# Performance work log

Measured on AMD Instinct MI355X. Metric: run time of the kernel, lower is better.

## Reference

```python
import jax, jax.numpy as jnp
import numpy as np

B, N, P = 256, 12, 66
DN = 1024   # node_feature_size
DE = 1024   # edge_feature_size
D = 512     # message_size
DIMS = [3 * D, 1024, 512]  # shared trunk dims; heads differ only in out classes
C_LR, C_CR, C_MR = 9, 3, 5


def _mlp(x, Ws, bs):
    # ReLU MLP, no activation on final layer (eval mode: dropout is identity)
    for i, (W, b) in enumerate(zip(Ws, bs)):
        x = x @ W + b
        if i < len(Ws) - 1:
            x = jax.nn.relu(x)
    return x


def _head_params(key, out_dim):
    dims = DIMS + [out_dim]
    Ws, bs = [], []
    for i in range(len(dims) - 1):
        key, k = jax.random.split(key)
        Ws.append(jax.random.normal(k, (dims[i], dims[i + 1]), jnp.float32) * (1.0 / np.sqrt(dims[i])))
        bs.append(jnp.zeros((dims[i + 1],), jnp.float32))
    return Ws, bs


def setup_inputs() -> dict:
    key = jax.random.key(0)
    ks = jax.random.split(key, 12)
    inp = {
        'node_features': jax.random.normal(ks[0], (B, N, DN), jnp.float32),
        'edge_features': jax.random.normal(ks[1], (B, N, N, DE), jnp.float32),
        'edge_embeddings': jax.random.normal(ks[2], (B, N, N, D), jnp.float32),
        'pairs': jax.random.randint(ks[3], (B, P, 2), 0, N),
        'num_rels': jax.random.randint(ks[4], (B,), 0, P + 1),
        'W_node': jax.random.normal(ks[5], (DN, D), jnp.float32) * (1.0 / np.sqrt(DN)),
        'b_node': jnp.zeros((D,), jnp.float32),
        'W_edge': jax.random.normal(ks[6], (DE, D), jnp.float32) * (1.0 / np.sqrt(DE)),
        'b_edge': jnp.zeros((D,), jnp.float32),
    }
    for name, cdim, k in (('lr', C_LR, ks[7]), ('cr', C_CR, ks[8]), ('mr', C_MR, ks[9])):
        Ws, bs = _head_params(k, cdim)
        for i in range(3):
            inp[f'{name}_W{i}'] = Ws[i]
            inp[f'{name}_b{i}'] = bs[i]
    return inp


def reference(node_features, edge_features, edge_embeddings, pairs, num_rels,
              W_node, b_node, W_edge, b_edge,
              lr_W0, lr_b0, lr_W1, lr_b1, lr_W2, lr_b2,
              cr_W0, cr_b0, cr_W1, cr_b1, cr_W2, cr_b2,
              mr_W0, mr_b0, mr_W1, mr_b1, mr_W2, mr_b2):
    # feature resize linears
    nf = node_features @ W_node + b_node        # [B,N,D]
    ef = edge_features @ W_edge + b_edge        # [B,N,N,D]

    # vectorized make_classifier_inputs
    i0, i1 = pairs[..., 0], pairs[..., 1]       # [B,P]
    bidx = jnp.arange(nf.shape[0])[:, None]     # [B,1]
    n1 = nf[bidx, i0]                           # [B,P,D]
    n2 = nf[bidx, i1]                           # [B,P,D]
    emb_mean = 0.5 * (edge_embeddings[bidx, i0, i1] + edge_embeddings[bidx, i1, i0])
    feat_mean = 0.5 * (ef[bidx, i0, i1] + ef[bidx, i1, i0])
    e = 0.5 * (emb_mean + feat_mean)            # [B,P,D]
    ci = jnp.concatenate([n1, n2, e], axis=-1)  # [B,P,3D]

    # rows i >= num_rels[b] stay zero (preallocated-zeros semantics)
    valid = (jnp.arange(ci.shape[1])[None, :] < num_rels[:, None])[..., None]
    ci = jnp.where(valid, ci, jnp.zeros((), ci.dtype))

    lr = _mlp(ci, [lr_W0, lr_W1, lr_W2], [lr_b0, lr_b1, lr_b2])
    cr = _mlp(ci, [cr_W0, cr_W1, cr_W2], [cr_b0, cr_b1, cr_b2])
    mr = _mlp(ci, [mr_W0, mr_W1, mr_W2], [mr_b0, mr_b1, mr_b2])
    return lr, cr, mr
```

## Files before the change

### kernel.cpp

```cpp
#include <hip/hip_runtime.h>
#include <stdint.h>

#define BB 256
#define NNODE 12
#define PP 66
#define DNF 1024
#define DEF 1024
#define DD 512
#define MROWS (BB*PP)
#define MNODE (BB*NNODE)
#define MTILES (MROWS/128)

typedef __attribute__((ext_vector_type(8))) short s16x8;
typedef __attribute__((ext_vector_type(4))) float f32x4;
typedef __attribute__((ext_vector_type(8))) unsigned short u16x8;

__device__ __forceinline__ unsigned short f2bf(float f) {
  union { float f; unsigned u; } v; v.f = f;
  return (unsigned short)((v.u + 0x7FFFu + ((v.u >> 16) & 1u)) >> 16);
}
__device__ __forceinline__ float bf2f(unsigned short h) {
  union { unsigned u; float f; } v; v.u = ((unsigned)h) << 16;
  return v.f;
}

__device__ __forceinline__ void gll16(const void* g, void* l) {
  __builtin_amdgcn_global_load_lds(
      (const __attribute__((address_space(1))) void*)g,
      (__attribute__((address_space(3))) void*)l, 16, 0, 0);
}

__global__ __launch_bounds__(256) void k_front(
    const int* __restrict__ nrels, int* __restrict__ offs,
    int* __restrict__ Mv, int2* __restrict__ nodes,
    float* __restrict__ h1part,
    const float* __restrict__ node, unsigned short* __restrict__ node_bf,
    const float* __restrict__ W_node, unsigned short* __restrict__ WnT,
    const float* __restrict__ W_edge, unsigned short* __restrict__ WeT,
    const float* __restrict__ W0a, const float* __restrict__ W0b,
    const float* __restrict__ W0c, unsigned short* __restrict__ W0T,
    const float* __restrict__ W1a, const float* __restrict__ W1b,
    const float* __restrict__ W1c, unsigned short* __restrict__ W1T,
    const float* __restrict__ w2a, const float* __restrict__ w2b,
    const float* __restrict__ w2c,
    const float* __restrict__ b2a, const float* __restrict__ b2b,
    const float* __restrict__ b2c,
    unsigned short* __restrict__ W2T, float* __restrict__ b2pad,
    const float* __restrict__ b0a, const float* __restrict__ b0b,
    const float* __restrict__ b0c, float* __restrict__ b0cat,
    const float* __restrict__ b1a, const float* __restrict__ b1b,
    const float* __restrict__ b1c, float* __restrict__ b1cat,
    const float* __restrict__ b_node, const float* __restrict__ b_edge,
    float* __restrict__ b_ne) {
  __shared__ float tile[64][65];
  const int bid = blockIdx.x, t = threadIdx.x;
  if (bid < 24) {
    const int h = bid >> 3, c = bid & 7;
    const float* b0 = h == 0 ? b0a : (h == 1 ? b0b : b0c);
    const float* W1 = h == 0 ? W1a : (h == 1 ? W1b : W1c);
    const int k0 = c * 128;
    float acc0 = 0.f, acc1 = 0.f;
#pragma unroll 8
    for (int kk = 0; kk < 128; ++kk) {
      const int k = k0 + kk;
      const float bv = fmaxf(b0[k], 0.f);
      acc0 += bv * W1[(size_t)k * 512 + t];
      acc1 += bv * W1[(size_t)k * 512 + t + 256];
    }
    h1part[(size_t)bid * 512 + t] = acc0;
    h1part[(size_t)bid * 512 + t + 256] = acc1;
  } else if (bid == 24) {
    __shared__ int s[256];
    const int val = nrels[t];
    s[t] = val;
    __syncthreads();
    for (int d = 1; d < 256; d <<= 1) {
      int x = (t >= d) ? s[t - d] : 0;
      __syncthreads();
      s[t] += x;
      __syncthreads();
    }
    offs[t] = s[t] - val;
    __syncthreads();
    const int total = s[255];
    if (t == 0) *Mv = total;
    if (t < 128) {
      int cr = total + t;
      if (cr < MROWS) nodes[cr] = make_int2(0, 0);
    }
  } else if (bid < 3097) {
    int i = (bid - 25) * 256 + t;
    float4 v = ((const float4*)node)[i];
    ushort4 o;
    o.x = f2bf(v.x); o.y = f2bf(v.y); o.z = f2bf(v.z); o.w = f2bf(v.w);
    ((ushort4*)node_bf)[i] = o;
  } else if (bid < 4889) {
    int tau = bid - 3097;
    const float* src; unsigned short* dst; int K, N;
    if (tau < 128)       { src = W_node; dst = WnT; K = 1024; N = 512; }
    else if (tau < 256)  { src = W_edge; dst = WeT; K = 1024; N = 512; tau -= 128; }
    else if (tau < 1408) {
      int hh = (tau - 256) / 384; tau = (tau - 256) % 384;
      src = hh == 0 ? W0a : (hh == 1 ? W0b : W0c);
      dst = W0T + (size_t)hh * 1024 * 1536; K = 1536; N = 1024;
    } else {
      int hh = (tau - 1408) / 128; tau = (tau - 1408) % 128;
      src = hh == 0 ? W1a : (hh == 1 ? W1b : W1c);
      dst = W1T + (size_t)hh * 512 * 1024; K = 1024; N = 512;
    }
    const int ntn = N >> 6;
    const int kb = (tau / ntn) * 64, nb = (tau % ntn) * 64;
    const int tx = t & 15, ty = t >> 4;
#pragma unroll
    for (int i = 0; i < 4; i++) {
      float4 v = *(const float4*)&src[(size_t)(kb + ty + 16 * i) * N + nb + tx * 4];
      tile[ty + 16 * i][tx * 4 + 0] = v.x;
      tile[ty + 16 * i][tx * 4 + 1] = v.y;
      tile[ty + 16 * i][tx * 4 + 2] = v.z;
      tile[ty + 16 * i][tx * 4 + 3] = v.w;
    }
    __syncthreads();
    const int wx = t & 7, wy = t >> 3;
#pragma unroll
    for (int i = 0; i < 2; i++) {
      const int n = wy + 32 * i;
      u16x8 o;
#pragma unroll
      for (int j = 0; j < 8; j++) o[j] = f2bf(tile[wx * 8 + j][n]);
      *(u16x8*)&dst[(size_t)(nb + n) * K + kb + wx * 8] = o;
    }
  } else if (bid < 5657) {
    int e = bid - 4889;
    int h = e >> 8, blk = e & 255;
    const int C = (h == 0) ? 9 : ((h == 1) ? 3 : 5);
    const float* W2 = (h == 0) ? w2a : ((h == 1) ? w2b : w2c);
    const float* b2 = (h == 0) ? b2a : ((h == 1) ? b2b : b2c);
    int idx = blk * 256 + t;
    int n = idx >> 9, k = idx & 511;
    W2T[(size_t)h * 65536 + idx] = (n < C) ? f2bf(W2[(size_t)k * C + n]) : (unsigned short)0;
    if (blk == 0 && t < 128)
      b2pad[h * 128 + t] = (t < C) ? b2[t] : 0.f;
  } else if (bid < 5669) {
    int j = bid - 5657;
    const float* b0 = (j < 4) ? b0a : (j < 8 ? b0b : b0c);
    b0cat[j * 256 + t] = b0[(j & 3) * 256 + t];
  } else if (bid < 5675) {
    int j = bid - 5669;
    const float* b1 = (j < 2) ? b1a : (j < 4 ? b1b : b1c);
    b1cat[j * 256 + t] = b1[(j & 1) * 256 + t];
  } else {
    int idx = (bid - 5675) * 256 + t;
    b_ne[idx] = (idx < 512) ? b_node[idx] : b_edge[idx - 512];
  }
}

template <int EPI>
__device__ __forceinline__ void gemm_body(
    unsigned short* sm,
    const unsigned short* __restrict__ A, int ldA,
    const unsigned short* __restrict__ BT, int ldB, int K,
    int Ntiles,
    const float* __restrict__ bias,
    unsigned short* __restrict__ outb, int ldo,
    const unsigned short* __restrict__ em,
    const int* __restrict__ Mvp,
    unsigned short* __restrict__ ci,
    int blocksPerHead, long long aHeadOff, long long bHeadOff,
    long long oHeadOff, int biasHeadOff,
    const int2* __restrict__ nodes,
    const unsigned short* __restrict__ nfa,
    const unsigned short* __restrict__ nfb,
    const int* __restrict__ rmap, int bid) {
  char* smc = (char*)sm;
  const int t = threadIdx.x;
  const int l = t & 63, w = t >> 6;
  const int wm = w >> 1, wn = w & 1;

  int head = 0;
  unsigned short* outp = outb;
  if constexpr (EPI == 3) {
    head = bid / MTILES;
    bid -= head * MTILES;
    A += (size_t)head * MROWS * DD;
    BT += (size_t)head * 128 * DD;
    bias += head * 128;
  } else {
    if (blocksPerHead > 0) {
      head = bid / blocksPerHead;
      bid -= head * blocksPerHead;
      A += (long long)head * aHeadOff;
      BT += (long long)head * bHeadOff;
      bias += head * biasHeadOff;
      outp = outb + (long long)head * oHeadOff;
    }
  }
  const int tn = bid % Ntiles, tm = bid / Ntiles;

  int Mv = MROWS;
  if (Mvp) {
    Mv = *Mvp;
    if (tm * 128 >= Mv) return;
  }

  const int lrow = l >> 3;
  const int scol = (l & 7) ^ lrow;
  const unsigned short* Ap = A + (size_t)(tm * 128 + w * 8 + lrow) * ldA + scol * 8;
  const unsigned short* Bp = BT + (size_t)(tn * 128 + w * 8 + lrow) * ldB + scol * 8;

  f32x4 acc[4][4] = {};
  const int hi = l >> 4, l15 = l & 15, l7 = l & 7;
  const int nk = K >> 6;

  for (int kt = 0; kt < nk; ++kt) {
#pragma unroll
    for (int c = 0; c < 4; ++c) {
      gll16(Ap + (size_t)c * 32 * ldA, smc + c * 4096 + w * 1024);
      gll16(Bp + (size_t)c * 32 * ldB, smc + 16384 + c * 4096 + w * 1024);
    }
    __syncthreads();
#pragma unroll
    for (int kk = 0; kk < 2; ++kk) {
      const int cb = (((kk << 2) + hi) ^ l7) << 4;
      s16x8 af[4], bfr[4];
#pragma unroll
      for (int m = 0; m < 4; m++)
        af[m] = *(const s16x8*)(smc + (wm * 64 + m * 16 + l15) * 128 + cb);
#pragma unroll
      for (int n = 0; n < 4; n++)
        bfr[n] = *(const s16x8*)(smc + 16384 + (wn * 64 + n * 16 + l15) * 128 + cb);
#pragma unroll
      for (int m = 0; m < 4; m++)
#pragma unroll
        for (int n = 0; n < 4; n++)
          asm volatile("v_mfma_f32_16x16x32_bf16 %0, %1, %2, %0"
                       : "+v"(acc[m][n])
                       : "v"(af[m]), "v"(bfr[n]));
    }
    __syncthreads();
    Ap += 64;
    Bp += 64;
  }
  asm volatile("s_nop 7\n\ts_nop 7\n\ts_nop 7" :::);

  if constexpr (EPI == 5) {
    const int se_r = t >> 4;
    const int se_ch = t & 15;
#pragma unroll
    for (int it = 0; it < 8; ++it) {
      const int rr = se_r + (it << 4);
      const int2 nn = nodes[tm * 128 + rr];
      union { unsigned short s[8]; unsigned long long q[2]; } ov;
      u16x8 va = *(const u16x8*)&nfa[(size_t)nn.x * 3072 + tn * 128 + se_ch * 8];
      u16x8 vb = *(const u16x8*)&nfb[(size_t)nn.y * 3072 + tn * 128 + se_ch * 8];
#pragma unroll
      for (int j = 0; j < 8; ++j)
        ov.s[j] = f2bf(bf2f(va[j]) + bf2f(vb[j]));
      const int sch = se_ch ^ ((rr >> 2) & 7);
      *(unsigned long long*)(smc + rr * 256 + (sch << 4)) = ov.q[0];
      *(unsigned long long*)(smc + rr * 256 + (sch << 4) + 8) = ov.q[1];
    }
    __syncthreads();
  }

  const int gr_base = tm * 128 + wm * 64 + (hi << 2);
  const int gc_base = tn * 128 + wn * 64 + l15;
  const int lr_base = wm * 64 + (hi << 2);
  const int lc_base = wn * 64 + l15;

  int Cc = 0; size_t obase = 0;
  if constexpr (EPI == 3) {
    Cc = (head == 0) ? 9 : ((head == 1) ? 3 : 5);
    obase = (head == 0) ? 0 : ((head == 1) ? (size_t)MROWS * 9 : (size_t)MROWS * 12);
  }

#pragma unroll
  for (int n = 0; n < 4; n++) {
    const int gc = gc_base + n * 16;
    const float bv = (EPI == 4) ? 0.f : bias[gc];
#pragma unroll
    for (int m = 0; m < 4; m++) {
#pragma unroll
      for (int i = 0; i < 4; i++) {
        const int gr = gr_base + m * 16 + i;
        float v = acc[m][n][i] + bv;
        if constexpr (EPI == 0 || EPI == 4) {
          outp[(size_t)gr * ldo + gc] = f2bf(v);
        } else if constexpr (EPI == 1) {
          float e = bf2f(em[(size_t)gr * DD + gc]) + 0.5f * v;
          ci[(size_t)gr * DD + gc] = f2bf(e);
        } else if constexpr (EPI == 2) {
          outp[(size_t)gr * ldo + gc] = f2bf(v > 0.f ? v : 0.f);
        } else if constexpr (EPI == 5) {
          const int lr = lr_base + m * 16 + i;
          const int lc = lc_base + n * 16;
          const int rch = (lc >> 3) ^ ((lr >> 2) & 7);
          v += bf2f(*(const unsigned short*)(smc + lr * 256 + (rch << 4) + (lc & 7) * 2));
          outp[(size_t)gr * ldo + gc] = f2bf(v > 0.f ? v : 0.f);
        } else {
          if (gc < Cc && gr < Mv)
            ((float*)outb)[obase + (size_t)rmap[gr] * Cc + gc] = v;
        }
      }
    }
  }
}

__global__ __launch_bounds__(256) void k_gather_nf(
    const float* __restrict__ EF, const float* __restrict__ EE,
    const int* __restrict__ pairs, const int* __restrict__ nrels,
    const int* __restrict__ offs,
    unsigned short* __restrict__ efm, unsigned short* __restrict__ emb,
    int2* __restrict__ nodes, int* __restrict__ rmap,
    const float* __restrict__ h1part,
    const float* __restrict__ b1a, const float* __restrict__ b1b,
    const float* __restrict__ b1c,
    const float* __restrict__ w2a, const float* __restrict__ w2b,
    const float* __restrict__ w2c,
    const float* __restrict__ b2a, const float* __restrict__ b2b,
    const float* __restrict__ b2c, float* __restrict__ outc,
    const unsigned short* __restrict__ node_bf,
    const unsigned short* __restrict__ WnT,
    const float* __restrict__ b_node, unsigned short* __restrict__ nf) {
  __shared__ __align__(16) unsigned short sm[16384];
  const int bid = blockIdx.x, t = threadIdx.x;
  if (bid > MROWS) {
    gemm_body<0>(sm, node_bf, 1024, WnT, 1024, 1024, 4, b_node, nf, 512,
                 nullptr, nullptr, nullptr, 0, 0, 0, 0, 0,
                 nullptr, nullptr, nullptr, nullptr, bid - MROWS - 1);
    return;
  }
  if (bid == MROWS) {
    float* red = (float*)sm;
    for (int h = 0; h < 3; ++h) {
      const float* b1 = h == 0 ? b1a : (h == 1 ? b1b : b1c);
      const float* W2 = h == 0 ? w2a : (h == 1 ? w2b : w2c);
      const float* b2 = h == 0 ? b2a : (h == 1 ? b2b : b2c);
      const int C = h == 0 ? 9 : (h == 1 ? 3 : 5);
      const int obase = h == 0 ? 0 : (h == 1 ? 9 : 12);
      if (t < 9) red[t] = 0.f;
      float s0 = b1[t], s1 = b1[t + 256];
#pragma unroll
      for (int cc = 0; cc < 8; ++cc) {
        s0 += h1part[(size_t)(h * 8 + cc) * 512 + t];
        s1 += h1part[(size_t)(h * 8 + cc) * 512 + t + 256];
      }
      const float hv0 = fmaxf(s0, 0.f), hv1 = fmaxf(s1, 0.f);
      __syncthreads();
      float p[9] = {0.f, 0.f, 0.f, 0.f, 0.f, 0.f, 0.f, 0.f, 0.f};
#pragma unroll
      for (int c = 0; c < 9; ++c)
        if (c < C) p[c] = hv0 * W2[(size_t)t * C + c] + hv1 * W2[(size_t)(t + 256) * C + c];
#pragma unroll
      for (int c = 0; c < 9; ++c)
#pragma unroll
        for (int off = 32; off; off >>= 1) p[c] += __shfl_xor(p[c], off);
      if ((t & 63) == 0)
        for (int c = 0; c < C; ++c) atomicAdd(&red[c], p[c]);
      __syncthreads();
      if (t < C) outc[obase + t] = red[t] + b2[t];
      __syncthreads();
    }
    return;
  }
  int r = bid;
  int b = r / PP, p = r - b * PP;
  if (p >= nrels[b]) return;
  const int cr = offs[b] + p;
  int i0 = pairs[r * 2 + 0], i1 = pairs[r * 2 + 1];
  if (t == 0) {
    nodes[cr] = make_int2(b * NNODE + i0, b * NNODE + i1);
    rmap[cr] = r;
  }
  const float4* e01 = (const float4*)(EF + ((size_t)((b * NNODE + i0) * NNODE + i1)) * DEF);
  const float4* e10 = (const float4*)(EF + ((size_t)((b * NNODE + i1) * NNODE + i0)) * DEF);
  float4 a = e01[t], c = e10[t];
  ushort4 o;
  o.x = f2bf(0.5f * (a.x + c.x));
  o.y = f2bf(0.5f * (a.y + c.y));
  o.z = f2bf(0.5f * (a.z + c.z));
  o.w = f2bf(0.5f * (a.w + c.w));
  ((ushort4*)(efm + (size_t)cr * DEF))[t] = o;
  const float2* g01 = (const float2*)(EE + ((size_t)((b * NNODE + i0) * NNODE + i1)) * DD);
  const float2* g10 = (const float2*)(EE + ((size_t)((b * NNODE + i1) * NNODE + i0)) * DD);
  float2 x = g01[t], y = g10[t];
  ushort2 eo;
  eo.x = f2bf(0.25f * (x.x + y.x));
  eo.y = f2bf(0.25f * (x.y + y.y));
  ((ushort2*)(emb + (size_t)cr * DD))[t] = eo;
}

__global__ __launch_bounds__(256) void k_mid(
    const unsigned short* __restrict__ efm, const unsigned short* __restrict__ WeT,
    const float* __restrict__ b_edge,
    const unsigned short* __restrict__ EMb, const int* __restrict__ Mvp,
    unsigned short* __restrict__ ci_e,
    const unsigned short* __restrict__ nf, const unsigned short* __restrict__ W0T,
    unsigned short* __restrict__ nfa,
    const float* __restrict__ outc, float* __restrict__ out) {
  __shared__ __align__(16) unsigned short sm[16384];
  const int bid = blockIdx.x, t = threadIdx.x;
  if (bid < 528) {
    gemm_body<1>(sm, efm, 1024, WeT, 1024, 1024, 4, b_edge, nullptr, 0,
                 EMb, Mvp, ci_e, 0, 0, 0, 0, 0,
                 nullptr, nullptr, nullptr, nullptr, bid);
  } else if (bid < 1680) {
    gemm_body<4>(sm, nf, 512, W0T, 1536, 512, 24, nullptr, nfa, 3072,
                 nullptr, nullptr, nullptr, 576,
                 0, 512, (long long)MNODE * 3072, 0,
                 nullptr, nullptr, nullptr, nullptr, bid - 528);
  } else {
    const int e = (bid - 1680) * 256 + t;
    if (e < MROWS * 17) {
      int c;
      if (e < MROWS * 9) c = e % 9;
      else if (e < MROWS * 12) c = 9 + (e - MROWS * 9) % 3;
      else c = 12 + (e - MROWS * 12) % 5;
      out[e] = outc[c];
    }
  }
}

template <int EPI>
__global__ __launch_bounds__(256) void k_gemm(
    const unsigned short* __restrict__ A, int ldA,
    const unsigned short* __restrict__ BT, int ldB, int K,
    int Ntiles,
    const float* __restrict__ bias,
    unsigned short* __restrict__ outb, int ldo,
    const unsigned short* __restrict__ em,
    const int* __restrict__ Mvp,
    unsigned short* __restrict__ ci,
    int blocksPerHead, long long aHeadOff, long long bHeadOff,
    long long oHeadOff, int biasHeadOff,
    const int2* __restrict__ nodes,
    const unsigned short* __restrict__ nfa,
    const unsigned short* __restrict__ nfb,
    const int* __restrict__ rmap) {
  __shared__ __align__(16) unsigned short sm[16384];
  gemm_body<EPI>(sm, A, ldA, BT, ldB, K, Ntiles, bias, outb, ldo, em, Mvp, ci,
                 blocksPerHead, aHeadOff, bHeadOff, oHeadOff, biasHeadOff,
                 nodes, nfa, nfb, rmap, blockIdx.x);
}

extern "C" void kernel_launch(void* const* d_in, const int* in_sizes, int n_in,
                              void* d_out, int out_size, void* d_ws, size_t ws_size,
                              hipStream_t stream) {
  const float* node   = (const float*)d_in[0];
  const float* EF     = (const float*)d_in[1];
  const float* EE     = (const float*)d_in[2];
  const int*   pairs  = (const int*)d_in[3];
  const int*   nrels  = (const int*)d_in[4];
  const float* W_node = (const float*)d_in[5];
  const float* b_node = (const float*)d_in[6];
  const float* W_edge = (const float*)d_in[7];
  const float* b_edge = (const float*)d_in[8];
  const float* hW0[3] = {(const float*)d_in[9],  (const float*)d_in[15], (const float*)d_in[21]};
  const float* hb0[3] = {(const float*)d_in[10], (const float*)d_in[16], (const float*)d_in[22]};
  const float* hW1[3] = {(const float*)d_in[11], (const float*)d_in[17], (const float*)d_in[23]};
  const float* hb1[3] = {(const float*)d_in[12], (const float*)d_in[18], (const float*)d_in[24]};
  const float* hW2[3] = {(const float*)d_in[13], (const float*)d_in[19], (const float*)d_in[25]};
  const float* hb2[3] = {(const float*)d_in[14], (const float*)d_in[20], (const float*)d_in[26]};

  char* ws = (char*)d_ws;
  size_t off = 0;
  auto alloc = [&](size_t bytes) {
    char* p = ws + off;
    off += (bytes + 255) & ~(size_t)255;
    return p;
  };
  unsigned short* WnT    = (unsigned short*)alloc((size_t)512 * 1024 * 2);
  unsigned short* WeT    = (unsigned short*)alloc((size_t)512 * 1024 * 2);
  unsigned short* W0T    = (unsigned short*)alloc((size_t)3072 * 1536 * 2);
  unsigned short* W1T    = (unsigned short*)alloc((size_t)3 * 512 * 1024 * 2);
  unsigned short* W2T    = (unsigned short*)alloc((size_t)3 * 128 * 512 * 2);
  float*          b2pad  = (float*)alloc((size_t)3 * 128 * 4);
  float*          b0cat  = (float*)alloc((size_t)3072 * 4);
  float*          b1cat  = (float*)alloc((size_t)1536 * 4);
  float*          b_ne   = (float*)alloc((size_t)1024 * 4);
  int2*           nodes  = (int2*)alloc((size_t)MROWS * 8);
  int*            offs   = (int*)alloc((size_t)256 * 4);
  int*            Mv     = (int*)alloc(256);
  int*            rmap   = (int*)alloc((size_t)MROWS * 4);
  float*          outc   = (float*)alloc((size_t)32 * 4);
  float*          h1part = (float*)alloc((size_t)24 * 512 * 4);
  size_t zoneB = off;
  unsigned short* ci_e = (unsigned short*)alloc((size_t)MROWS * DD * 2);
  unsigned short* nfa  = (unsigned short*)alloc((size_t)MNODE * 3072 * 2);
  unsigned short* nfb  = (unsigned short*)alloc((size_t)MNODE * 3072 * 2);
  size_t zoneC = off;
  unsigned short* node_bf = (unsigned short*)alloc((size_t)MNODE * DNF * 2);
  unsigned short* nf      = (unsigned short*)alloc((size_t)MNODE * DD * 2);
  unsigned short* efm     = (unsigned short*)alloc((size_t)MROWS * DEF * 2);
  unsigned short* EMb     = (unsigned short*)alloc((size_t)MROWS * DD * 2);
  unsigned short* h1    = (unsigned short*)(ws + zoneB);
  unsigned short* h0big = (unsigned short*)(ws + zoneC);

  k_front<<<5679, 256, 0, stream>>>(nrels, offs, Mv, nodes, h1part,
      node, node_bf, W_node, WnT, W_edge, WeT,
      hW0[0], hW0[1], hW0[2], W0T, hW1[0], hW1[1], hW1[2], W1T,
      hW2[0], hW2[1], hW2[2], hb2[0], hb2[1], hb2[2], W2T, b2pad,
      hb0[0], hb0[1], hb0[2], b0cat, hb1[0], hb1[1], hb1[2], b1cat,
      b_node, b_edge, b_ne);

  k_gather_nf<<<MROWS + 1 + (MNODE / 128) * 4, 256, 0, stream>>>(
      EF, EE, pairs, nrels, offs, efm, EMb, nodes, rmap, h1part,
      hb1[0], hb1[1], hb1[2], hW2[0], hW2[1], hW2[2],
      hb2[0], hb2[1], hb2[2], outc,
      node_bf, WnT, b_ne, nf);

  k_mid<<<1680 + (MROWS * 17 + 255) / 256, 256, 0, stream>>>(
      efm, WeT, b_ne + 512, EMb, Mv, ci_e,
      nf, W0T, nfa, outc, (float*)d_out);

  k_gemm<5><<<MTILES * 24, 256, 0, stream>>>(
      ci_e, 512, W0T + 1024, 1536, 512, 24, b0cat, h0big, 3072,
      nullptr, Mv, nullptr, 0, 0, 0, 0, 0, nodes, nfa, nfb, nullptr);

  k_gemm<2><<<3 * MTILES * 4, 256, 0, stream>>>(
      h0big, 3072, W1T, 1024, 1024, 4, b1cat, h1, 512,
      nullptr, Mv, nullptr, MTILES * 4,
      1024, (long long)512 * 1024, (long long)MROWS * DD, 512,
      nullptr, nullptr, nullptr, nullptr);

  k_gemm<3><<<3 * MTILES, 256, 0, stream>>>(
      h1, 512, W2T, 512, 512, 1, b2pad, (unsigned short*)d_out, 0,
      nullptr, Mv, nullptr, 0, 0, 0, 0, 0, nullptr, nullptr, nullptr, rmap);
}
```

Measured before the change: 198.8 us.

## Fuse three layer-2 heads into one block-diagonal GEMM and move output fill

Layer-1 outputs of the three heads are now written side by side into one [M,1536] buffer. The final layer runs as a single GEMM over K=1536 against a block-diagonal W2T that packs all 17 classes into one 128-wide tile, replacing three per-head launches. The epilogue routes each column to its head's output slice. The constant-output fill moves out of k_mid into a new kernel that also runs the layer-0 GEMM. This trades three small K=512 GEMMs for one launch with three times the K work, most of which multiplies zeros.

```diff
diff --git a/kernel.cpp b/kernel.cpp
--- a/kernel.cpp
+++ b/kernel.cpp
@@ -130,16 +130,25 @@
       *(u16x8*)&dst[(size_t)(nb + n) * K + kb + wx * 8] = o;
     }
   } else if (bid < 5657) {
-    int e = bid - 4889;
-    int h = e >> 8, blk = e & 255;
-    const int C = (h == 0) ? 9 : ((h == 1) ? 3 : 5);
-    const float* W2 = (h == 0) ? w2a : ((h == 1) ? w2b : w2c);
-    const float* b2 = (h == 0) ? b2a : ((h == 1) ? b2b : b2c);
-    int idx = blk * 256 + t;
-    int n = idx >> 9, k = idx & 511;
-    W2T[(size_t)h * 65536 + idx] = (n < C) ? f2bf(W2[(size_t)k * C + n]) : (unsigned short)0;
-    if (blk == 0 && t < 128)
-      b2pad[h * 128 + t] = (t < C) ? b2[t] : 0.f;
+    const int blk = bid - 4889;
+    const int idx = blk * 256 + t;
+    const int n = idx / 1536, k = idx - n * 1536;
+    unsigned short v = 0;
+    if (n < 9) {
+      if (k < 512) v = f2bf(w2a[(size_t)k * 9 + n]);
+    } else if (n < 12) {
+      if (k >= 512 && k < 1024) v = f2bf(w2b[(size_t)(k - 512) * 3 + (n - 9)]);
+    } else if (n < 17) {
+      if (k >= 1024) v = f2bf(w2c[(size_t)(k - 1024) * 5 + (n - 12)]);
+    }
+    W2T[idx] = v;
+    if (blk == 0 && t < 128) {
+      float bv = 0.f;
+      if (t < 9) bv = b2a[t];
+      else if (t < 12) bv = b2b[t - 9];
+      else if (t < 17) bv = b2c[t - 12];
+      b2pad[t] = bv;
+    }
   } else if (bid < 5669) {
     int j = bid - 5657;
     const float* b0 = (j < 4) ? b0a : (j < 8 ? b0b : b0c);
@@ -178,21 +187,13 @@
 
   int head = 0;
   unsigned short* outp = outb;
-  if constexpr (EPI == 3) {
-    head = bid / MTILES;
-    bid -= head * MTILES;
-    A += (size_t)head * MROWS * DD;
-    BT += (size_t)head * 128 * DD;
-    bias += head * 128;
-  } else {
-    if (blocksPerHead > 0) {
-      head = bid / blocksPerHead;
-      bid -= head * blocksPerHead;
-      A += (long long)head * aHeadOff;
-      BT += (long long)head * bHeadOff;
-      bias += head * biasHeadOff;
-      outp = outb + (long long)head * oHeadOff;
-    }
+  if (blocksPerHead > 0) {
+    head = bid / blocksPerHead;
+    bid -= head * blocksPerHead;
+    A += (long long)head * aHeadOff;
+    BT += (long long)head * bHeadOff;
+    bias += head * biasHeadOff;
+    outp = outb + (long long)head * oHeadOff;
   }
   const int tn = bid % Ntiles, tm = bid / Ntiles;
 
@@ -266,12 +267,6 @@
   const int gc_base = tn * 128 + wn * 64 + l15;
   const int lr_base = wm * 64 + (hi << 2);
   const int lc_base = wn * 64 + l15;
-
-  int Cc = 0; size_t obase = 0;
-  if constexpr (EPI == 3) {
-    Cc = (head == 0) ? 9 : ((head == 1) ? 3 : 5);
-    obase = (head == 0) ? 0 : ((head == 1) ? (size_t)MROWS * 9 : (size_t)MROWS * 12);
-  }
 
 #pragma unroll
   for (int n = 0; n < 4; n++) {
@@ -297,8 +292,14 @@
           v += bf2f(*(const unsigned short*)(smc + lr * 256 + (rch << 4) + (lc & 7) * 2));
           outp[(size_t)gr * ldo + gc] = f2bf(v > 0.f ? v : 0.f);
         } else {
-          if (gc < Cc && gr < Mv)
-            ((float*)outb)[obase + (size_t)rmap[gr] * Cc + gc] = v;
+          if (gc < 17 && gr < Mv) {
+            const int hh = gc < 9 ? 0 : (gc < 12 ? 1 : 2);
+            const int Ch = hh == 0 ? 9 : (hh == 1 ? 3 : 5);
+            const int cc = gc - (hh == 0 ? 0 : (hh == 1 ? 9 : 12));
+            const size_t ob = hh == 0 ? 0
+                             : (hh == 1 ? (size_t)MROWS * 9 : (size_t)MROWS * 12);
+            ((float*)outb)[ob + (size_t)rmap[gr] * Ch + cc] = v;
+          }
         }
       }
     }
@@ -395,21 +396,34 @@
     const unsigned short* __restrict__ EMb, const int* __restrict__ Mvp,
     unsigned short* __restrict__ ci_e,
     const unsigned short* __restrict__ nf, const unsigned short* __restrict__ W0T,
-    unsigned short* __restrict__ nfa,
-    const float* __restrict__ outc, float* __restrict__ out) {
+    unsigned short* __restrict__ nfa) {
   __shared__ __align__(16) unsigned short sm[16384];
-  const int bid = blockIdx.x, t = threadIdx.x;
+  const int bid = blockIdx.x;
   if (bid < 528) {
     gemm_body<1>(sm, efm, 1024, WeT, 1024, 1024, 4, b_edge, nullptr, 0,
                  EMb, Mvp, ci_e, 0, 0, 0, 0, 0,
                  nullptr, nullptr, nullptr, nullptr, bid);
-  } else if (bid < 1680) {
+  } else {
     gemm_body<4>(sm, nf, 512, W0T, 1536, 512, 24, nullptr, nfa, 3072,
                  nullptr, nullptr, nullptr, 576,
                  0, 512, (long long)MNODE * 3072, 0,
                  nullptr, nullptr, nullptr, nullptr, bid - 528);
-  } else {
-    const int e = (bid - 1680) * 256 + t;
+  }
+}
+
+__global__ __launch_bounds__(256) void k_l0(
+    const unsigned short* __restrict__ ci_e,
+    const unsigned short* __restrict__ W0Te,
+    const float* __restrict__ b0cat,
+    unsigned short* __restrict__ h0big,
+    const int* __restrict__ Mvp, const int2* __restrict__ nodes,
+    const unsigned short* __restrict__ nfa,
+    const unsigned short* __restrict__ nfb,
+    const float* __restrict__ outc, float* __restrict__ out) {
+  __shared__ __align__(16) unsigned short sm[16384];
+  const int bid = blockIdx.x, t = threadIdx.x;
+  if (bid < 1122) {
+    const int e = bid * 256 + t;
     if (e < MROWS * 17) {
       int c;
       if (e < MROWS * 9) c = e % 9;
@@ -417,7 +431,11 @@
       else c = 12 + (e - MROWS * 12) % 5;
       out[e] = outc[c];
     }
-  }
+    return;
+  }
+  gemm_body<5>(sm, ci_e, 512, W0Te, 1536, 512, 24, b0cat, h0big, 3072,
+               nullptr, Mvp, nullptr, 0, 0, 0, 0, 0,
+               nodes, nfa, nfb, nullptr, bid - 1122);
 }
 
 template <int EPI>
@@ -472,8 +490,8 @@
   unsigned short* WeT    = (unsigned short*)alloc((size_t)512 * 1024 * 2);
   unsigned short* W0T    = (unsigned short*)alloc((size_t)3072 * 1536 * 2);
   unsigned short* W1T    = (unsigned short*)alloc((size_t)3 * 512 * 1024 * 2);
-  unsigned short* W2T    = (unsigned short*)alloc((size_t)3 * 128 * 512 * 2);
-  float*          b2pad  = (float*)alloc((size_t)3 * 128 * 4);
+  unsigned short* W2T    = (unsigned short*)alloc((size_t)128 * 1536 * 2);
+  float*          b2pad  = (float*)alloc((size_t)128 * 4);
   float*          b0cat  = (float*)alloc((size_t)3072 * 4);
   float*          b1cat  = (float*)alloc((size_t)1536 * 4);
   float*          b_ne   = (float*)alloc((size_t)1024 * 4);
@@ -508,21 +526,20 @@
       hb2[0], hb2[1], hb2[2], outc,
       node_bf, WnT, b_ne, nf);
 
-  k_mid<<<1680 + (MROWS * 17 + 255) / 256, 256, 0, stream>>>(
-      efm, WeT, b_ne + 512, EMb, Mv, ci_e,
-      nf, W0T, nfa, outc, (float*)d_out);
-
-  k_gemm<5><<<MTILES * 24, 256, 0, stream>>>(
-      ci_e, 512, W0T + 1024, 1536, 512, 24, b0cat, h0big, 3072,
-      nullptr, Mv, nullptr, 0, 0, 0, 0, 0, nodes, nfa, nfb, nullptr);
+  k_mid<<<1680, 256, 0, stream>>>(
+      efm, WeT, b_ne + 512, EMb, Mv, ci_e, nf, W0T, nfa);
+
+  k_l0<<<1122 + MTILES * 24, 256, 0, stream>>>(
+      ci_e, W0T + 1024, b0cat, h0big, Mv, nodes, nfa, nfb,
+      outc, (float*)d_out);
 
   k_gemm<2><<<3 * MTILES * 4, 256, 0, stream>>>(
-      h0big, 3072, W1T, 1024, 1024, 4, b1cat, h1, 512,
+      h0big, 3072, W1T, 1024, 1024, 4, b1cat, h1, 1536,
       nullptr, Mv, nullptr, MTILES * 4,
-      1024, (long long)512 * 1024, (long long)MROWS * DD, 512,
+      1024, (long long)512 * 1024, 512, 512,
       nullptr, nullptr, nullptr, nullptr);
 
-  k_gemm<3><<<3 * MTILES, 256, 0, stream>>>(
-      h1, 512, W2T, 512, 512, 1, b2pad, (unsigned short*)d_out, 0,
+  k_gemm<3><<<MTILES, 256, 0, stream>>>(
+      h1, 1536, W2T, 1536, 1536, 1, b2pad, (unsigned short*)d_out, 0,
       nullptr, Mv, nullptr, 0, 0, 0, 0, 0, nullptr, nullptr, nullptr, rmap);
 }
```

New measurement: 215.3 us. +8.3%, slower.
